# Optimization experiments

Hardware: AMD Instinct MI355X
Metric: run time of the kernel (lower is better)

The kernel has to match this reference:

```python
import jax, jax.numpy as jnp
import numpy as np

EMB_DIM = 64
B, S, D = 64, 1024, 64

def setup_inputs() -> dict:
    key = jax.random.key(0)
    k1, k2, k3, k4, k5 = jax.random.split(key, 5)
    return {
        "query": jax.random.normal(k1, (B, S, D), dtype=jnp.float32),
        "key": jax.random.normal(k2, (B, S, D), dtype=jnp.float32),
        "value": jax.random.normal(k3, (B, S, D), dtype=jnp.float32),
        "a_key": jax.random.normal(k4, (S, S, D), dtype=jnp.float32),
        "a_value": jax.random.normal(k5, (S, S, D), dtype=jnp.float32),
    }

def reference(query, key, value, a_key, a_value):
    scale = jnp.sqrt(jnp.asarray(EMB_DIM, dtype=query.dtype))
    # standard content-content scores: [B, Sq, Sk]
    qk = jnp.einsum("bqd,bkd->bqk", query, key)
    # relative key scores: a_key is [Sq, Sk, D]; contract over D per query position
    rel_qk = jnp.einsum("bqd,qkd->bqk", query, a_key)
    attn = jax.nn.softmax((qk + rel_qk) / scale, axis=-1)
    # content values + relative values
    qkv = jnp.einsum("bqk,bkd->bqd", attn, value)
    rel_qkv = jnp.einsum("bqk,qkd->bqd", attn, a_value)
    return qkv + rel_qkv, attn
```

## Files before the change

### kernel.cpp

```cpp
#include <hip/hip_runtime.h>
#include <stdint.h>

#define S_ 1024
#define D_ 64
#define B_ 64

typedef short short8 __attribute__((ext_vector_type(8)));
typedef unsigned short ushort8 __attribute__((ext_vector_type(8)));
typedef float f32x4 __attribute__((ext_vector_type(4)));

__device__ __forceinline__ unsigned short f2bf(float x) {
    uint32_t u = __builtin_bit_cast(uint32_t, x);
    return (unsigned short)((u + 0x7FFFu + ((u >> 16) & 1u)) >> 16);
}
__device__ __forceinline__ float bf2f(unsigned short b) {
    return __builtin_bit_cast(float, ((uint32_t)b) << 16);
}
__device__ __forceinline__ uint32_t pack2(float a, float b) {
    return (uint32_t)f2bf(a) | ((uint32_t)f2bf(b) << 16);
}
__device__ __forceinline__ short8 mkfrag(float4 a, float4 b) {
    union { short8 s; uint32_t u[4]; } r;
    r.u[0] = pack2(a.x, a.y); r.u[1] = pack2(a.z, a.w);
    r.u[2] = pack2(b.x, b.y); r.u[3] = pack2(b.z, b.w);
    return r.s;
}
__device__ __forceinline__ int scidx(int row, int k) {
    return (((row << 10) + (k & ~7)) ^ ((row & 15) << 3)) + (k & 7);
}

__global__ __launch_bounds__(256) void k1_qk(const float* __restrict__ Q,
                                             const float* __restrict__ Kk,
                                             float* __restrict__ qk) {
    __shared__ __align__(16) unsigned short Qs[128][72];
    __shared__ __align__(16) unsigned short Ks[128][72];
    const float SCL = 0.18033688011112042f;
    const int bx = blockIdx.x;
    const int b  = bx >> 6;
    const int q0 = ((bx >> 3) & 7) << 7;
    const int k0 = (bx & 7) << 7;
    const int t  = threadIdx.x;
#pragma unroll
    for (int i = 0; i < 8; ++i) {
        int f = (i << 8) + t;
        int row = f >> 4, c = (f & 15) << 2;
        float4 v = *reinterpret_cast<const float4*>(&Q[((size_t)(b * S_ + q0 + row) << 6) + c]);
        *reinterpret_cast<uint2*>(&Qs[row][c]) = make_uint2(pack2(v.x, v.y), pack2(v.z, v.w));
        float4 u = *reinterpret_cast<const float4*>(&Kk[((size_t)(b * S_ + k0 + row) << 6) + c]);
        *reinterpret_cast<uint2*>(&Ks[row][c]) = make_uint2(pack2(u.x, u.y), pack2(u.z, u.w));
    }
    __syncthreads();
    const int l = t & 63, w = t >> 6, lr = l & 15, lg = l >> 4;
    short8 a[2][2];
#pragma unroll
    for (int mi = 0; mi < 2; ++mi)
#pragma unroll
        for (int h = 0; h < 2; ++h)
            a[mi][h] = *reinterpret_cast<const short8*>(&Qs[((w * 2 + mi) << 4) + lr][h * 32 + lg * 8]);
    f32x4 acc[2][8] = {};
#pragma unroll
    for (int n = 0; n < 8; ++n) {
        short8 b0 = *reinterpret_cast<const short8*>(&Ks[(n << 4) + lr][lg * 8]);
        short8 b1 = *reinterpret_cast<const short8*>(&Ks[(n << 4) + lr][32 + lg * 8]);
#pragma unroll
        for (int mi = 0; mi < 2; ++mi) {
            acc[mi][n] = __builtin_amdgcn_mfma_f32_16x16x32_bf16(a[mi][0], b0, acc[mi][n], 0, 0, 0);
            acc[mi][n] = __builtin_amdgcn_mfma_f32_16x16x32_bf16(a[mi][1], b1, acc[mi][n], 0, 0, 0);
        }
    }
#pragma unroll
    for (int mi = 0; mi < 2; ++mi)
#pragma unroll
        for (int n = 0; n < 8; ++n)
#pragma unroll
            for (int r = 0; r < 4; ++r) {
                int qq = q0 + ((w * 2 + mi) << 4) + (lg << 2) + r;
                int kc = k0 + (n << 4) + lr;
                qk[((size_t)(b * S_ + qq) << 10) + kc] = acc[mi][n][r] * SCL;
            }
}

__device__ __forceinline__ void tpose_store_p(unsigned short* Tls, int pitch, float4 p,
                                              int kb, int t) {
    const int l = t & 63, lr = l & 15, lg = l >> 4;
    float v0 = p.x, v1 = p.y, v2 = p.z, v3 = p.w;
    float y0 = __shfl_xor(v0, 16), y1 = __shfl_xor(v1, 16),
          y2 = __shfl_xor(v2, 16), y3 = __shfl_xor(v3, 16);
    bool o = (lg & 1);
    float n0 = o ? y1 : v0, n1 = o ? v1 : y0, n2 = o ? y3 : v2, n3 = o ? v3 : y2;
    float z0 = __shfl_xor(n0, 32), z1 = __shfl_xor(n1, 32),
          z2 = __shfl_xor(n2, 32), z3 = __shfl_xor(n3, 32);
    bool h = (lg & 2);
    float T0 = h ? z2 : n0, T1 = h ? z3 : n1, T2 = h ? n2 : z0, T3 = h ? n3 : z1;
    int d = (lr << 2) + lg;
    *reinterpret_cast<uint2*>(&Tls[d * pitch + kb]) = make_uint2(pack2(T0, T1), pack2(T2, T3));
}

__global__ __launch_bounds__(512) void k2_mid(const float* __restrict__ Q,
                                              const float* __restrict__ AK,
                                              const float* __restrict__ AV,
                                              float* __restrict__ attn,
                                              float* __restrict__ outp) {
    __shared__ __align__(16) unsigned short Sc[64 * 1024];
    __shared__ __align__(16) unsigned short Qs[64][72];
    __shared__ __align__(16) unsigned short Ak[2][64][72];
    __shared__ float invs[64];
    const float SCL = 0.18033688011112042f;
    const int q = blockIdx.x;
    const int t = threadIdx.x;
    const int l = t & 63, w = t >> 6, lr = l & 15, lg = l >> 4;
    const int wq = w & 3;
    const int th = w >> 2;
    const int srow = t >> 3, sc8 = (t & 7) << 3;

    {
        const float* qp = &Q[((size_t)(srow * S_ + q) << 6) + sc8];
        float4 a = *reinterpret_cast<const float4*>(qp);
        float4 b = *reinterpret_cast<const float4*>(qp + 4);
        *reinterpret_cast<uint4*>(&Qs[srow][sc8]) =
            make_uint4(pack2(a.x * SCL, a.y * SCL), pack2(a.z * SCL, a.w * SCL),
                       pack2(b.x * SCL, b.y * SCL), pack2(b.z * SCL, b.w * SCL));
    }
    __syncthreads();
    short8 qa[4][2];
#pragma unroll
    for (int bh = 0; bh < 4; ++bh)
#pragma unroll
        for (int h = 0; h < 2; ++h)
            qa[bh][h] = *reinterpret_cast<const short8*>(
                &Qs[(bh << 4) + lr][(h << 5) + (lg << 3)]);

    {
        const float* base = &AK[((size_t)q << 16) + (((wq << 4) + lr) << 6) + (lg << 3)];
        float4 A0[2], A1[2], A2[2], A3[2];
#define LDA(buf, i8) do { const float* p_ = base + ((size_t)((th << 3) + (i8)) << 12); \
        A0[buf] = *reinterpret_cast<const float4*>(p_);                                \
        A1[buf] = *reinterpret_cast<const float4*>(p_ + 4);                            \
        A2[buf] = *reinterpret_cast<const float4*>(p_ + 32);                           \
        A3[buf] = *reinterpret_cast<const float4*>(p_ + 36); } while (0)
        LDA(0, 0); LDA(1, 1);
#pragma unroll 2
        for (int i8 = 0; i8 < 8; ++i8) {
            const int buf = i8 & 1;
            short8 ak0 = mkfrag(A0[buf], A1[buf]);
            short8 ak1 = mkfrag(A2[buf], A3[buf]);
            if (i8 < 6) LDA(buf, i8 + 2);
            int kbase = (((th << 3) + i8) << 6) + (wq << 4) + (lg << 2);
#pragma unroll
            for (int bh = 0; bh < 4; ++bh) {
                f32x4 c = {};
                c = __builtin_amdgcn_mfma_f32_16x16x32_bf16(ak0, qa[bh][0], c, 0, 0, 0);
                c = __builtin_amdgcn_mfma_f32_16x16x32_bf16(ak1, qa[bh][1], c, 0, 0, 0);
                *reinterpret_cast<uint2*>(&Sc[scidx((bh << 4) + lr, kbase)]) =
                    make_uint2(pack2(c[0], c[1]), pack2(c[2], c[3]));
            }
        }
#undef LDA
    }
    __syncthreads();

    const float* avbase = &AV[(size_t)q << 16];
    float4 pv[2][2];
#pragma unroll
    for (int s = 0; s < 2; ++s)
#pragma unroll
        for (int i = 0; i < 2; ++i) {
            int f = (i << 9) + t;
            pv[s][i] = *reinterpret_cast<const float4*>(
                &avbase[((size_t)s << 12) + ((size_t)(f >> 4) << 6) + ((f & 15) << 2)]);
        }

    {
        const int ch = t & 7;
        const float* qkrow = &attn[((size_t)(srow * S_ + q) << 10)];
        float s = 0.f;
#pragma unroll 4
        for (int i = 0; i < 16; ++i) {
            int k = (((i << 3) + ch) << 3);
            float4 g0 = *reinterpret_cast<const float4*>(&qkrow[k]);
            float4 g1 = *reinterpret_cast<const float4*>(&qkrow[k + 4]);
            int idx = scidx(srow, k);
            ushort8 rel = *reinterpret_cast<const ushort8*>(&Sc[idx]);
            float p0 = exp2f(g0.x + bf2f(rel[0]));
            float p1 = exp2f(g0.y + bf2f(rel[1]));
            float p2 = exp2f(g0.z + bf2f(rel[2]));
            float p3 = exp2f(g0.w + bf2f(rel[3]));
            float p4 = exp2f(g1.x + bf2f(rel[4]));
            float p5 = exp2f(g1.y + bf2f(rel[5]));
            float p6 = exp2f(g1.z + bf2f(rel[6]));
            float p7 = exp2f(g1.w + bf2f(rel[7]));
            s += ((p0 + p1) + (p2 + p3)) + ((p4 + p5) + (p6 + p7));
            ushort8 e;
            e[0] = f2bf(p0); e[1] = f2bf(p1); e[2] = f2bf(p2); e[3] = f2bf(p3);
            e[4] = f2bf(p4); e[5] = f2bf(p5); e[6] = f2bf(p6); e[7] = f2bf(p7);
            *reinterpret_cast<ushort8*>(&Sc[idx]) = e;
        }
        s += __shfl_xor(s, 1); s += __shfl_xor(s, 2); s += __shfl_xor(s, 4);
        if (ch == 0) invs[srow] = 1.0f / s;
    }
    __syncthreads();

    tpose_store_p(&Ak[0][0][0], 72, pv[0][0], (w << 2), t);
    tpose_store_p(&Ak[0][0][0], 72, pv[0][1], 32 + (w << 2), t);
    __syncthreads();

    f32x4 oacc[2] = {};
#pragma unroll 2
    for (int tt = 0; tt < 16; ++tt) {
        const int cur = tt & 1, nxt = cur ^ 1;
        short8 bb0 = *reinterpret_cast<const short8*>(&Ak[cur][(wq << 4) + lr][lg << 3]);
        short8 bb1 = *reinterpret_cast<const short8*>(&Ak[cur][(wq << 4) + lr][32 + (lg << 3)]);
        if (tt < 15) {
            tpose_store_p(&Ak[nxt][0][0], 72, pv[nxt][0], (w << 2), t);
            tpose_store_p(&Ak[nxt][0][0], 72, pv[nxt][1], 32 + (w << 2), t);
        }
        if (tt < 14) {
#pragma unroll
            for (int i = 0; i < 2; ++i) {
                int f = (i << 9) + t;
                pv[cur][i] = *reinterpret_cast<const float4*>(
                    &avbase[((size_t)(tt + 2) << 12) + ((size_t)(f >> 4) << 6) + ((f & 15) << 2)]);
            }
        }
        {
            int col = (t & 255) << 2;
#pragma unroll
            for (int rr = 0; rr < 2; ++rr) {
                int row = (tt << 2) + (rr << 1) + th;
                uint2 u = *reinterpret_cast<const uint2*>(&Sc[scidx(row, col)]);
                float inv = invs[row];
                float4 o = make_float4(bf2f((unsigned short)(u.x & 0xffff)) * inv,
                                       bf2f((unsigned short)(u.x >> 16)) * inv,
                                       bf2f((unsigned short)(u.y & 0xffff)) * inv,
                                       bf2f((unsigned short)(u.y >> 16)) * inv);
                *reinterpret_cast<float4*>(&attn[((size_t)(row * S_ + q) << 10) + col]) = o;
            }
        }
#pragma unroll
        for (int mi = 0; mi < 2; ++mi) {
            short8 ea0 = *reinterpret_cast<const short8*>(
                &Sc[scidx((th << 5) + (mi << 4) + lr, (tt << 6) + (lg << 3))]);
            short8 ea1 = *reinterpret_cast<const short8*>(
                &Sc[scidx((th << 5) + (mi << 4) + lr, (tt << 6) + 32 + (lg << 3))]);
            oacc[mi] = __builtin_amdgcn_mfma_f32_16x16x32_bf16(ea0, bb0, oacc[mi], 0, 0, 0);
            oacc[mi] = __builtin_amdgcn_mfma_f32_16x16x32_bf16(ea1, bb1, oacc[mi], 0, 0, 0);
        }
        __syncthreads();
    }
#pragma unroll
    for (int mi = 0; mi < 2; ++mi)
#pragma unroll
        for (int r = 0; r < 4; ++r) {
            int brow = (th << 5) + (mi << 4) + (lg << 2) + r;
            outp[((size_t)(brow * S_ + q) << 6) + (wq << 4) + lr] = oacc[mi][r] * invs[brow];
        }
}

__global__ __launch_bounds__(512) void k3_pv(const float* __restrict__ V,
                                             const float* __restrict__ attn,
                                             float* __restrict__ outp) {
    __shared__ __align__(16) unsigned short Vt[64 * 1032];
    const int b  = blockIdx.x >> 2;
    const int qq = blockIdx.x & 3;
    const int t  = threadIdx.x;
    const int l = t & 63, w = t >> 6, lr = l & 15, lg = l >> 4;
    const int wq = w & 3;
    const int dh = w >> 2;

    for (int kt = 0; kt < 16; ++kt) {
#pragma unroll
        for (int i = 0; i < 2; ++i) {
            int f = (i << 9) + t;
            int row = f >> 4, c = (f & 15) << 2;
            float4 pvv = *reinterpret_cast<const float4*>(
                &V[((size_t)(b * S_ + (kt << 6) + row) << 6) + c]);
            tpose_store_p(&Vt[0], 1032, pvv, (kt << 6) + (i << 5) + (w << 2), t);
        }
    }
    __syncthreads();

    for (int qs = 0; qs < 4; ++qs) {
        const float* arow = &attn[((size_t)((b * S_ + (qq << 8) + (qs << 6) + (wq << 4) + lr)) << 10) + (lg << 3)];
        float4 A0[2], A1[2], A2[2], A3[2];
#define LDP(buf, kt) do { const float* p_ = arow + ((kt) << 6);        \
        A0[buf] = *reinterpret_cast<const float4*>(p_);                \
        A1[buf] = *reinterpret_cast<const float4*>(p_ + 4);            \
        A2[buf] = *reinterpret_cast<const float4*>(p_ + 32);           \
        A3[buf] = *reinterpret_cast<const float4*>(p_ + 36); } while (0)
        LDP(0, 0); LDP(1, 1);
        f32x4 acc[2] = {};
#pragma unroll 2
        for (int kt = 0; kt < 16; ++kt) {
            const int buf = kt & 1;
            short8 a0 = mkfrag(A0[buf], A1[buf]);
            short8 a1 = mkfrag(A2[buf], A3[buf]);
            if (kt < 14) LDP(buf, kt + 2);
#pragma unroll
            for (int n = 0; n < 2; ++n) {
                const unsigned short* vb = &Vt[((dh << 5) + (n << 4) + lr) * 1032 + (kt << 6) + (lg << 3)];
                short8 b0 = *reinterpret_cast<const short8*>(vb);
                short8 b1 = *reinterpret_cast<const short8*>(vb + 32);
                acc[n] = __builtin_amdgcn_mfma_f32_16x16x32_bf16(a0, b0, acc[n], 0, 0, 0);
                acc[n] = __builtin_amdgcn_mfma_f32_16x16x32_bf16(a1, b1, acc[n], 0, 0, 0);
            }
        }
#undef LDP
#pragma unroll
        for (int n = 0; n < 2; ++n)
#pragma unroll
            for (int r = 0; r < 4; ++r) {
                size_t idx = ((size_t)(b * S_ + (qq << 8) + (qs << 6) + (wq << 4) + (lg << 2) + r) << 6)
                             + (dh << 5) + (n << 4) + lr;
                outp[idx] += acc[n][r];
            }
    }
}

extern "C" void kernel_launch(void* const* d_in, const int* in_sizes, int n_in,
                              void* d_out, int out_size, void* d_ws, size_t ws_size,
                              hipStream_t stream) {
    (void)in_sizes; (void)n_in; (void)out_size; (void)d_ws; (void)ws_size;
    const float* Q  = (const float*)d_in[0];
    const float* K  = (const float*)d_in[1];
    const float* V  = (const float*)d_in[2];
    const float* AK = (const float*)d_in[3];
    const float* AV = (const float*)d_in[4];
    float* outp = (float*)d_out;
    float* attn = outp + (size_t)B_ * S_ * D_;

    k1_qk <<<dim3(64 * 8 * 8), dim3(256), 0, stream>>>(Q, K, attn);
    k2_mid<<<dim3(1024),       dim3(512), 0, stream>>>(Q, AK, AV, attn, outp);
    k3_pv <<<dim3(256),        dim3(512), 0, stream>>>(V, attn, outp);
}
```

Measured before the change: 415.0 us.

## Double block size to 1024 threads in k2_mid and k3_pv, redistributing per-thread work

Both the mid kernel and the PV kernel move from 512 to 1024 threads per block. Per-thread work is halved throughout: the AK tile loop, the softmax row chunks, the AV staging, the attn writeback and the MFMA output tiles, and k3 splits its query sub-tiles across wave groups. The goal is more waves per block to hide memory latency, since the large LDS footprint (~128KB for k2) limits each CU to one block. The trade-off is higher register pressure under 1024-thread launch bounds and more threads contending at each __syncthreads.

```diff
diff --git a/kernel.cpp b/kernel.cpp
--- a/kernel.cpp
+++ b/kernel.cpp
@@ -96,11 +96,11 @@
     *reinterpret_cast<uint2*>(&Tls[d * pitch + kb]) = make_uint2(pack2(T0, T1), pack2(T2, T3));
 }
 
-__global__ __launch_bounds__(512) void k2_mid(const float* __restrict__ Q,
-                                              const float* __restrict__ AK,
-                                              const float* __restrict__ AV,
-                                              float* __restrict__ attn,
-                                              float* __restrict__ outp) {
+__global__ __launch_bounds__(1024) void k2_mid(const float* __restrict__ Q,
+                                               const float* __restrict__ AK,
+                                               const float* __restrict__ AV,
+                                               float* __restrict__ attn,
+                                               float* __restrict__ outp) {
     __shared__ __align__(16) unsigned short Sc[64 * 1024];
     __shared__ __align__(16) unsigned short Qs[64][72];
     __shared__ __align__(16) unsigned short Ak[2][64][72];
@@ -110,16 +110,14 @@
     const int t = threadIdx.x;
     const int l = t & 63, w = t >> 6, lr = l & 15, lg = l >> 4;
     const int wq = w & 3;
-    const int th = w >> 2;
-    const int srow = t >> 3, sc8 = (t & 7) << 3;
+    const int wg = w >> 2;
+    const int srow = t >> 4, c4 = (t & 15) << 2;
 
     {
-        const float* qp = &Q[((size_t)(srow * S_ + q) << 6) + sc8];
+        const float* qp = &Q[((size_t)(srow * S_ + q) << 6) + c4];
         float4 a = *reinterpret_cast<const float4*>(qp);
-        float4 b = *reinterpret_cast<const float4*>(qp + 4);
-        *reinterpret_cast<uint4*>(&Qs[srow][sc8]) =
-            make_uint4(pack2(a.x * SCL, a.y * SCL), pack2(a.z * SCL, a.w * SCL),
-                       pack2(b.x * SCL, b.y * SCL), pack2(b.z * SCL, b.w * SCL));
+        *reinterpret_cast<uint2*>(&Qs[srow][c4]) =
+            make_uint2(pack2(a.x * SCL, a.y * SCL), pack2(a.z * SCL, a.w * SCL));
     }
     __syncthreads();
     short8 qa[4][2];
@@ -133,19 +131,19 @@
     {
         const float* base = &AK[((size_t)q << 16) + (((wq << 4) + lr) << 6) + (lg << 3)];
         float4 A0[2], A1[2], A2[2], A3[2];
-#define LDA(buf, i8) do { const float* p_ = base + ((size_t)((th << 3) + (i8)) << 12); \
+#define LDA(buf, i4) do { const float* p_ = base + ((size_t)((wg << 2) + (i4)) << 12); \
         A0[buf] = *reinterpret_cast<const float4*>(p_);                                \
         A1[buf] = *reinterpret_cast<const float4*>(p_ + 4);                            \
         A2[buf] = *reinterpret_cast<const float4*>(p_ + 32);                           \
         A3[buf] = *reinterpret_cast<const float4*>(p_ + 36); } while (0)
         LDA(0, 0); LDA(1, 1);
 #pragma unroll 2
-        for (int i8 = 0; i8 < 8; ++i8) {
-            const int buf = i8 & 1;
+        for (int i4 = 0; i4 < 4; ++i4) {
+            const int buf = i4 & 1;
             short8 ak0 = mkfrag(A0[buf], A1[buf]);
             short8 ak1 = mkfrag(A2[buf], A3[buf]);
-            if (i8 < 6) LDA(buf, i8 + 2);
-            int kbase = (((th << 3) + i8) << 6) + (wq << 4) + (lg << 2);
+            if (i4 < 2) LDA(buf, i4 + 2);
+            int kbase = (((wg << 2) + i4) << 6) + (wq << 4) + (lg << 2);
 #pragma unroll
             for (int bh = 0; bh < 4; ++bh) {
                 f32x4 c = {};
@@ -160,23 +158,19 @@
     __syncthreads();
 
     const float* avbase = &AV[(size_t)q << 16];
-    float4 pv[2][2];
+    float4 pv[2];
 #pragma unroll
     for (int s = 0; s < 2; ++s)
-#pragma unroll
-        for (int i = 0; i < 2; ++i) {
-            int f = (i << 9) + t;
-            pv[s][i] = *reinterpret_cast<const float4*>(
-                &avbase[((size_t)s << 12) + ((size_t)(f >> 4) << 6) + ((f & 15) << 2)]);
-        }
+        pv[s] = *reinterpret_cast<const float4*>(
+            &avbase[((size_t)s << 12) + ((size_t)srow << 6) + c4]);
 
     {
-        const int ch = t & 7;
+        const int ch = t & 15;
         const float* qkrow = &attn[((size_t)(srow * S_ + q) << 10)];
         float s = 0.f;
 #pragma unroll 4
-        for (int i = 0; i < 16; ++i) {
-            int k = (((i << 3) + ch) << 3);
+        for (int i = 0; i < 8; ++i) {
+            int k = (((i << 4) + ch) << 3);
             float4 g0 = *reinterpret_cast<const float4*>(&qkrow[k]);
             float4 g1 = *reinterpret_cast<const float4*>(&qkrow[k + 4]);
             int idx = scidx(srow, k);
@@ -195,91 +189,73 @@
             e[4] = f2bf(p4); e[5] = f2bf(p5); e[6] = f2bf(p6); e[7] = f2bf(p7);
             *reinterpret_cast<ushort8*>(&Sc[idx]) = e;
         }
-        s += __shfl_xor(s, 1); s += __shfl_xor(s, 2); s += __shfl_xor(s, 4);
+        s += __shfl_xor(s, 1); s += __shfl_xor(s, 2);
+        s += __shfl_xor(s, 4); s += __shfl_xor(s, 8);
         if (ch == 0) invs[srow] = 1.0f / s;
     }
     __syncthreads();
 
-    tpose_store_p(&Ak[0][0][0], 72, pv[0][0], (w << 2), t);
-    tpose_store_p(&Ak[0][0][0], 72, pv[0][1], 32 + (w << 2), t);
-    __syncthreads();
-
-    f32x4 oacc[2] = {};
+    tpose_store_p(&Ak[0][0][0], 72, pv[0], (w << 2), t);
+    __syncthreads();
+
+    f32x4 oacc = {};
 #pragma unroll 2
     for (int tt = 0; tt < 16; ++tt) {
         const int cur = tt & 1, nxt = cur ^ 1;
         short8 bb0 = *reinterpret_cast<const short8*>(&Ak[cur][(wq << 4) + lr][lg << 3]);
         short8 bb1 = *reinterpret_cast<const short8*>(&Ak[cur][(wq << 4) + lr][32 + (lg << 3)]);
-        if (tt < 15) {
-            tpose_store_p(&Ak[nxt][0][0], 72, pv[nxt][0], (w << 2), t);
-            tpose_store_p(&Ak[nxt][0][0], 72, pv[nxt][1], 32 + (w << 2), t);
-        }
-        if (tt < 14) {
-#pragma unroll
-            for (int i = 0; i < 2; ++i) {
-                int f = (i << 9) + t;
-                pv[cur][i] = *reinterpret_cast<const float4*>(
-                    &avbase[((size_t)(tt + 2) << 12) + ((size_t)(f >> 4) << 6) + ((f & 15) << 2)]);
-            }
-        }
+        if (tt < 15) tpose_store_p(&Ak[nxt][0][0], 72, pv[nxt], (w << 2), t);
+        if (tt < 14)
+            pv[cur] = *reinterpret_cast<const float4*>(
+                &avbase[((size_t)(tt + 2) << 12) + ((size_t)srow << 6) + c4]);
         {
             int col = (t & 255) << 2;
-#pragma unroll
-            for (int rr = 0; rr < 2; ++rr) {
-                int row = (tt << 2) + (rr << 1) + th;
-                uint2 u = *reinterpret_cast<const uint2*>(&Sc[scidx(row, col)]);
-                float inv = invs[row];
-                float4 o = make_float4(bf2f((unsigned short)(u.x & 0xffff)) * inv,
-                                       bf2f((unsigned short)(u.x >> 16)) * inv,
-                                       bf2f((unsigned short)(u.y & 0xffff)) * inv,
-                                       bf2f((unsigned short)(u.y >> 16)) * inv);
-                *reinterpret_cast<float4*>(&attn[((size_t)(row * S_ + q) << 10) + col]) = o;
-            }
-        }
-#pragma unroll
-        for (int mi = 0; mi < 2; ++mi) {
-            short8 ea0 = *reinterpret_cast<const short8*>(
-                &Sc[scidx((th << 5) + (mi << 4) + lr, (tt << 6) + (lg << 3))]);
-            short8 ea1 = *reinterpret_cast<const short8*>(
-                &Sc[scidx((th << 5) + (mi << 4) + lr, (tt << 6) + 32 + (lg << 3))]);
-            oacc[mi] = __builtin_amdgcn_mfma_f32_16x16x32_bf16(ea0, bb0, oacc[mi], 0, 0, 0);
-            oacc[mi] = __builtin_amdgcn_mfma_f32_16x16x32_bf16(ea1, bb1, oacc[mi], 0, 0, 0);
-        }
+            int row = (tt << 2) + (t >> 8);
+            uint2 u = *reinterpret_cast<const uint2*>(&Sc[scidx(row, col)]);
+            float inv = invs[row];
+            float4 o = make_float4(bf2f((unsigned short)(u.x & 0xffff)) * inv,
+                                   bf2f((unsigned short)(u.x >> 16)) * inv,
+                                   bf2f((unsigned short)(u.y & 0xffff)) * inv,
+                                   bf2f((unsigned short)(u.y >> 16)) * inv);
+            *reinterpret_cast<float4*>(&attn[((size_t)(row * S_ + q) << 10) + col]) = o;
+        }
+        short8 ea0 = *reinterpret_cast<const short8*>(
+            &Sc[scidx((wg << 4) + lr, (tt << 6) + (lg << 3))]);
+        short8 ea1 = *reinterpret_cast<const short8*>(
+            &Sc[scidx((wg << 4) + lr, (tt << 6) + 32 + (lg << 3))]);
+        oacc = __builtin_amdgcn_mfma_f32_16x16x32_bf16(ea0, bb0, oacc, 0, 0, 0);
+        oacc = __builtin_amdgcn_mfma_f32_16x16x32_bf16(ea1, bb1, oacc, 0, 0, 0);
         __syncthreads();
     }
 #pragma unroll
-    for (int mi = 0; mi < 2; ++mi)
-#pragma unroll
-        for (int r = 0; r < 4; ++r) {
-            int brow = (th << 5) + (mi << 4) + (lg << 2) + r;
-            outp[((size_t)(brow * S_ + q) << 6) + (wq << 4) + lr] = oacc[mi][r] * invs[brow];
-        }
-}
-
-__global__ __launch_bounds__(512) void k3_pv(const float* __restrict__ V,
-                                             const float* __restrict__ attn,
-                                             float* __restrict__ outp) {
+    for (int r = 0; r < 4; ++r) {
+        int brow = (wg << 4) + (lg << 2) + r;
+        outp[((size_t)(brow * S_ + q) << 6) + (wq << 4) + lr] = oacc[r] * invs[brow];
+    }
+}
+
+__global__ __launch_bounds__(1024) void k3_pv(const float* __restrict__ V,
+                                              const float* __restrict__ attn,
+                                              float* __restrict__ outp) {
     __shared__ __align__(16) unsigned short Vt[64 * 1032];
     const int b  = blockIdx.x >> 2;
     const int qq = blockIdx.x & 3;
     const int t  = threadIdx.x;
     const int l = t & 63, w = t >> 6, lr = l & 15, lg = l >> 4;
     const int wq = w & 3;
-    const int dh = w >> 2;
+    const int dh = (w >> 2) & 1;
+    const int qg = w >> 3;
 
     for (int kt = 0; kt < 16; ++kt) {
-#pragma unroll
-        for (int i = 0; i < 2; ++i) {
-            int f = (i << 9) + t;
-            int row = f >> 4, c = (f & 15) << 2;
-            float4 pvv = *reinterpret_cast<const float4*>(
-                &V[((size_t)(b * S_ + (kt << 6) + row) << 6) + c]);
-            tpose_store_p(&Vt[0], 1032, pvv, (kt << 6) + (i << 5) + (w << 2), t);
-        }
-    }
-    __syncthreads();
-
-    for (int qs = 0; qs < 4; ++qs) {
+        float4 pvv = *reinterpret_cast<const float4*>(
+            &V[((size_t)(b * S_ + (kt << 6) + (t >> 4)) << 6) + ((t & 15) << 2)]);
+        tpose_store_p(&Vt[0], 1032, pvv, (kt << 6) + (w << 2), t);
+    }
+    __syncthreads();
+
+#pragma unroll
+    for (int qs2 = 0; qs2 < 2; ++qs2) {
+        const int qs = (qg << 1) + qs2;
         const float* arow = &attn[((size_t)((b * S_ + (qq << 8) + (qs << 6) + (wq << 4) + lr)) << 10) + (lg << 3)];
         float4 A0[2], A1[2], A2[2], A3[2];
 #define LDP(buf, kt) do { const float* p_ = arow + ((kt) << 6);        \
@@ -328,7 +304,7 @@
     float* outp = (float*)d_out;
     float* attn = outp + (size_t)B_ * S_ * D_;
 
-    k1_qk <<<dim3(64 * 8 * 8), dim3(256), 0, stream>>>(Q, K, attn);
-    k2_mid<<<dim3(1024),       dim3(512), 0, stream>>>(Q, AK, AV, attn, outp);
-    k3_pv <<<dim3(256),        dim3(512), 0, stream>>>(V, attn, outp);
-}
+    k1_qk <<<dim3(64 * 8 * 8), dim3(256),  0, stream>>>(Q, K, attn);
+    k2_mid<<<dim3(1024),       dim3(1024), 0, stream>>>(Q, AK, AV, attn, outp);
+    k3_pv <<<dim3(256),        dim3(1024), 0, stream>>>(V, attn, outp);
+}
```

New measurement: 424.8 us. 2.3% more time.
